# Kernel optimization log

Hardware: AMD Instinct MI355X
Metric: run time of the kernel (lower is better)

The kernel has to match this reference:

```python
import jax, jax.numpy as jnp
import numpy as np

C = 256
CQK = C // 8  # query/key projection dim (in_dim // 8)
B, H, W = 4, 64, 64


def setup_inputs() -> dict:
    key = jax.random.key(0)
    ks = jax.random.split(key, 7)
    scale = 0.05
    x = jax.random.normal(ks[0], (B, C, H, W), dtype=jnp.float32)
    Wq = jax.random.normal(ks[1], (CQK, C), dtype=jnp.float32) * scale
    bq = jax.random.normal(ks[2], (CQK,), dtype=jnp.float32) * scale
    Wk = jax.random.normal(ks[3], (CQK, C), dtype=jnp.float32) * scale
    bk = jax.random.normal(ks[4], (CQK,), dtype=jnp.float32) * scale
    Wv = jax.random.normal(ks[5], (C, C), dtype=jnp.float32) * scale
    bv = jax.random.normal(ks[6], (C,), dtype=jnp.float32) * scale
    return {"x": x, "Wq": Wq, "bq": bq, "Wk": Wk, "bk": bk, "Wv": Wv, "bv": bv}


def reference(x, Wq, bq, Wk, bk, Wv, bv):
    b, c, h, w = x.shape
    n = h * w
    xf = x.reshape(b, c, n)  # [B, C, N]
    # 1x1 convs == per-pixel linear maps over channels
    q = jnp.einsum('dc,bcn->bnd', Wq, xf) + bq[None, None, :]   # [B, N, C/8]
    k = jnp.einsum('dc,bcn->bdn', Wk, xf) + bk[None, :, None]   # [B, C/8, N]
    v = jnp.einsum('dc,bcn->bdn', Wv, xf) + bv[None, :, None]   # [B, C, N]
    energy = jnp.einsum('bnd,bdm->bnm', q, k)                    # [B, N, N]
    attention = jax.nn.softmax(energy, axis=-1)                  # softmax over keys
    # out = V @ attention^T  (torch: bmm(proj_value, attention.permute(0,2,1)))
    out = jnp.einsum('bdm,bnm->bdn', v, attention)               # [B, C, N]
    return out.reshape(b, c, h, w) + x
```

## Files before the change

### kernel.cpp

```cpp
#include <hip/hip_runtime.h>
#include <math.h>

#define BATCH 4
#define CH    256
#define NPIX  4096
#define DQK   32

typedef short          s16;
typedef unsigned int   uint_t;
typedef __attribute__((ext_vector_type(8))) short short8;
typedef __attribute__((ext_vector_type(4))) float floatx4;
typedef __attribute__((ext_vector_type(16))) float floatx16;

__device__ __forceinline__ s16 f2bf(float f) {
  union { float f; uint_t u; } v; v.f = f;
  return (s16)((v.u + 0x8000u) >> 16);
}
__device__ __forceinline__ uint_t pk2(float a, float b) {
  union { float f; uint_t u; } x, y; x.f = a; y.f = b;
  return (((y.u + 0x8000u) >> 16) << 16) | ((x.u + 0x8000u) >> 16);
}

__global__ __launch_bounds__(256) void prepack(
    const float* __restrict__ Wq, const float* __restrict__ bq,
    const float* __restrict__ Wk, const float* __restrict__ bk,
    const float* __restrict__ Wv, const float* __restrict__ bv,
    s16* __restrict__ Wbf, float* __restrict__ Bsw)
{
  const int gid = blockIdx.x * 256 + threadIdx.x;
  const int e0  = gid * 4;
  const int row = e0 >> 8, col = e0 & 255;
  const float* src = (row < 32) ? Wq + (size_t)row * 256
                   : (row < 64) ? Wk + (size_t)(row - 32) * 256
                                : Wv + (size_t)(row - 64) * 256;
  float4 f = *(const float4*)(src + col);
  uint2 o; o.x = pk2(f.x, f.y); o.y = pk2(f.z, f.w);
  *(uint2*)(Wbf + e0) = o;
  if (gid < 320)
    Bsw[gid] = (gid < 32) ? bq[gid] : (gid < 64) ? bk[gid - 32] : bv[gid - 64];
}

__global__ __launch_bounds__(256, 2) void proj_mfma(
    const float* __restrict__ x, const s16* __restrict__ Wbf,
    const float* __restrict__ Bsw,
    s16* __restrict__ Qw, s16* __restrict__ Kw, s16* __restrict__ Vw)
{
  const int b  = blockIdx.x >> 7;
  const int n0 = (blockIdx.x & 127) << 5;
  const int t  = threadIdx.x;

  __shared__ s16 Xs[32][264];
  __shared__ s16 Os[256][40];

  const float* xb = x + (size_t)b * CH * NPIX + n0;
  #pragma unroll
  for (int i = 0; i < 2; ++i) {
    int task = i * 256 + t;
    int ncg  = task & 7;
    int kcg  = task >> 3;
    const float* src = xb + (size_t)(kcg * 4) * NPIX + ncg * 4;
    float rows[4][4];
    *(float4*)&rows[0][0] = *(const float4*)(src);
    *(float4*)&rows[1][0] = *(const float4*)(src + NPIX);
    *(float4*)&rows[2][0] = *(const float4*)(src + 2 * NPIX);
    *(float4*)&rows[3][0] = *(const float4*)(src + 3 * NPIX);
    #pragma unroll
    for (int c = 0; c < 4; ++c) {
      uint2 pk;
      pk.x = pk2(rows[0][c], rows[1][c]);
      pk.y = pk2(rows[2][c], rows[3][c]);
      *(uint2*)&Xs[ncg * 4 + c][kcg * 4] = pk;
    }
  }
  __syncthreads();

  const int w    = t >> 6;
  const int l15  = t & 15;
  const int quad = (t & 63) >> 4;

  floatx4 acc[5][2];
  #pragma unroll
  for (int si = 0; si < 5; ++si)
    #pragma unroll
    for (int nt = 0; nt < 2; ++nt) acc[si][nt] = (floatx4){0.f, 0.f, 0.f, 0.f};

  short8 afc[5], afn[5];
  #pragma unroll
  for (int si = 0; si < 5; ++si) {
    const int s = w + si * 4;
    afc[si] = *(const short8*)(Wbf + (size_t)(s * 16 + l15) * 256 + quad * 8);
  }
  for (int kc = 0; kc < 8; ++kc) {
    const int k0  = kc * 32;
    const int kn0 = (kc < 7) ? k0 + 32 : 0;
    #pragma unroll
    for (int si = 0; si < 5; ++si) {
      const int s = w + si * 4;
      afn[si] = *(const short8*)(Wbf + (size_t)(s * 16 + l15) * 256 + kn0 + quad * 8);
    }
    short8 bf[2];
    #pragma unroll
    for (int nt = 0; nt < 2; ++nt)
      bf[nt] = *(const short8*)&Xs[l15 + 16 * nt][k0 + quad * 8];
    #pragma unroll
    for (int si = 0; si < 5; ++si)
      #pragma unroll
      for (int nt = 0; nt < 2; ++nt)
        acc[si][nt] = __builtin_amdgcn_mfma_f32_16x16x32_bf16(afc[si], bf[nt], acc[si][nt], 0, 0, 0);
    #pragma unroll
    for (int si = 0; si < 5; ++si) afc[si] = afn[si];
  }

  #pragma unroll
  for (int si = 0; si < 5; ++si) {
    const int s = w + si * 4;
    float4 bb = *(const float4*)(Bsw + 16 * s + quad * 4);
    #pragma unroll
    for (int nt = 0; nt < 2; ++nt) {
      const int px  = 16 * nt + l15;
      float v0 = acc[si][nt][0] + bb.x;
      float v1 = acc[si][nt][1] + bb.y;
      float v2 = acc[si][nt][2] + bb.z;
      float v3 = acc[si][nt][3] + bb.w;
      if (s < 4) {
        s16* dst = (s < 2) ? Qw : Kw;
        int d0 = (s & 1) * 16 + quad * 4;
        uint2 pq; pq.x = pk2(v0, v1); pq.y = pk2(v2, v3);
        *(uint2*)(dst + ((size_t)b * NPIX + n0 + px) * DQK + d0) = pq;
      } else {
        const int c0 = (s - 4) * 16 + quad * 4;
        Os[c0 + 0][px] = f2bf(v0);
        Os[c0 + 1][px] = f2bf(v1);
        Os[c0 + 2][px] = f2bf(v2);
        Os[c0 + 3][px] = f2bf(v3);
      }
    }
  }
  __syncthreads();
  #pragma unroll
  for (int rep = 0; rep < 4; ++rep) {
    const int task = rep * 256 + t;
    const int ch   = task >> 2;
    const int seg  = task & 3;
    *(uint4*)(Vw + ((size_t)b * CH + ch) * NPIX + n0 + seg * 8) =
        *(const uint4*)&Os[ch][seg * 8];
  }
}

__global__ __launch_bounds__(512, 2) void attn_mfma(
    const s16* __restrict__ Qw, const s16* __restrict__ Kw,
    const s16* __restrict__ Vw, const float* __restrict__ x,
    float* __restrict__ out)
{
  const int bi = blockIdx.x;
  const int b  = bi & 3;
  const int qt = bi >> 2;
  const int n0 = qt * 64;
  const int t  = threadIdx.x;
  const int w    = t >> 6;
  const int l15  = t & 15;
  const int quad = (t & 63) >> 4;
  const int l31  = t & 31;
  const int lh   = (t & 63) >> 5;
  const int l7   = t & 7;
  const int cb   = 32 * w;

  __shared__ s16  Pt[2][64][128];
  __shared__ float Lsum[64][8];

  const s16* qbase = Qw + ((size_t)b * NPIX + n0) * DQK;
  short8 qb[4];
  #pragma unroll
  for (int tq = 0; tq < 4; ++tq)
    qb[tq] = *(const short8*)(qbase + (size_t)(16 * tq + l15) * DQK + quad * 8);

  floatx16 o[2];
  #pragma unroll
  for (int i = 0; i < 16; ++i) { o[0][i] = 0.f; o[1][i] = 0.f; }
  float l_part[4] = {0.f, 0.f, 0.f, 0.f};

  const s16* kbase = Kw + (size_t)b * NPIX * DQK;
  const s16* vbase = Vw + ((size_t)b * CH + cb) * NPIX;

  short8 ka_c, ka_n, va[8];
  ka_c = *(const short8*)(kbase + (size_t)(16 * w + l15) * DQK + quad * 8);
  #pragma unroll
  for (int ks = 0; ks < 8; ++ks)
    va[ks] = *(const short8*)(vbase + (size_t)l31 * NPIX + 16 * ks + 8 * lh);

  int buf = 0;
  for (int kt = 0; kt < 32; ++kt) {
    const int m0  = kt * 128;
    const int mn0 = (kt < 31) ? m0 + 128 : 0;

    floatx4 sacc[4];
    #pragma unroll
    for (int tq = 0; tq < 4; ++tq)
      sacc[tq] = __builtin_amdgcn_mfma_f32_16x16x32_bf16(
                   ka_c, qb[tq], (floatx4){0.f, 0.f, 0.f, 0.f}, 0, 0, 0);

    ka_n = *(const short8*)(kbase + (size_t)(mn0 + 16 * w + l15) * DQK + quad * 8);

    const int wslot = (((2 * w + (quad >> 1)) ^ l7) << 3) + (quad & 1) * 4;
    #pragma unroll
    for (int tq = 0; tq < 4; ++tq) {
      float p0 = __expf(fminf(sacc[tq][0], 60.f));
      float p1 = __expf(fminf(sacc[tq][1], 60.f));
      float p2 = __expf(fminf(sacc[tq][2], 60.f));
      float p3 = __expf(fminf(sacc[tq][3], 60.f));
      l_part[tq] += (p0 + p1) + (p2 + p3);
      uint2 pk; pk.x = pk2(p0, p1); pk.y = pk2(p2, p3);
      *(uint2*)&Pt[buf][16 * tq + l15][wslot] = pk;
    }
    __syncthreads();

    #pragma unroll
    for (int ks = 0; ks < 8; ++ks) {
      const int rslot = ((2 * ks + lh) ^ l7) << 3;
      short8 pb0 = *(const short8*)&Pt[buf][l31     ][rslot];
      short8 pb1 = *(const short8*)&Pt[buf][32 + l31][rslot];
      o[0] = __builtin_amdgcn_mfma_f32_32x32x16_bf16(va[ks], pb0, o[0], 0, 0, 0);
      o[1] = __builtin_amdgcn_mfma_f32_32x32x16_bf16(va[ks], pb1, o[1], 0, 0, 0);
    }
    #pragma unroll
    for (int ks = 0; ks < 8; ++ks)
      va[ks] = *(const short8*)(vbase + (size_t)l31 * NPIX + mn0 + 16 * ks + 8 * lh);

    ka_c = ka_n;
    buf ^= 1;
  }

  #pragma unroll
  for (int tq = 0; tq < 4; ++tq) {
    l_part[tq] += __shfl_xor(l_part[tq], 16);
    l_part[tq] += __shfl_xor(l_part[tq], 32);
  }
  if (quad == 0) {
    #pragma unroll
    for (int tq = 0; tq < 4; ++tq) Lsum[16 * tq + l15][w] = l_part[tq];
  }
  __syncthreads();

  #pragma unroll
  for (int half = 0; half < 2; ++half) {
    const int q = half * 32 + l31;
    float4 s0 = *(const float4*)&Lsum[q][0];
    float4 s1 = *(const float4*)&Lsum[q][4];
    float invq = 1.f / (((s0.x + s0.y) + (s0.z + s0.w)) +
                        ((s1.x + s1.y) + (s1.z + s1.w)));
    const int npx = n0 + q;
    #pragma unroll
    for (int r = 0; r < 16; ++r) {
      const int c = cb + (r & 3) + 8 * (r >> 2) + 4 * lh;
      const size_t off = ((size_t)b * CH + c) * NPIX + npx;
      out[off] = fmaf(o[half][r], invq, x[off]);
    }
  }
}

extern "C" void kernel_launch(void* const* d_in, const int* in_sizes, int n_in,
                              void* d_out, int out_size, void* d_ws, size_t ws_size,
                              hipStream_t stream) {
  (void)in_sizes; (void)n_in; (void)out_size; (void)ws_size;
  const float* x  = (const float*)d_in[0];
  const float* Wq = (const float*)d_in[1];
  const float* bq = (const float*)d_in[2];
  const float* Wk = (const float*)d_in[3];
  const float* bk = (const float*)d_in[4];
  const float* Wv = (const float*)d_in[5];
  const float* bv = (const float*)d_in[6];
  float* out = (float*)d_out;

  unsigned char* ws = (unsigned char*)d_ws;
  s16*   Qw  = (s16*)ws;
  s16*   Kw  = (s16*)(ws + (size_t)1 * 1024 * 1024);
  s16*   Vw  = (s16*)(ws + (size_t)2 * 1024 * 1024);
  s16*   Wbf = (s16*)(ws + (size_t)10 * 1024 * 1024);
  float* Bsw = (float*)(ws + (size_t)10 * 1024 * 1024 + 256 * 1024);

  hipLaunchKernelGGL(prepack, dim3(80), dim3(256), 0, stream,
                     Wq, bq, Wk, bk, Wv, bv, Wbf, Bsw);
  hipLaunchKernelGGL(proj_mfma, dim3(512), dim3(256), 0, stream,
                     x, Wbf, Bsw, Qw, Kw, Vw);
  hipLaunchKernelGGL(attn_mfma, dim3(256), dim3(512), 0, stream,
                     Qw, Kw, Vw, x, out);
}
```

Measured before the change: 158.1 us.

## Pre-tile V into MFMA fragment layout and split attention across 16 waves

```diff
diff --git a/kernel.cpp b/kernel.cpp
--- a/kernel.cpp
+++ b/kernel.cpp
@@ -140,16 +140,20 @@
   #pragma unroll
   for (int rep = 0; rep < 4; ++rep) {
     const int task = rep * 256 + t;
-    const int ch   = task >> 2;
-    const int seg  = task & 3;
-    *(uint4*)(Vw + ((size_t)b * CH + ch) * NPIX + n0 + seg * 8) =
-        *(const uint4*)&Os[ch][seg * 8];
-  }
-}
-
-__global__ __launch_bounds__(512, 2) void attn_mfma(
+    const int fid  = task >> 6;
+    const int ln   = task & 63;
+    const int c    = fid >> 1;
+    const int sl   = fid & 1;
+    const int row  = c * 32 + (ln & 31);
+    const int col  = sl * 16 + (ln >> 5) * 8;
+    *(uint4*)(Vw + (((size_t)b * 8 + c) * 256 + (n0 >> 4) + sl) * 512 + ln * 8) =
+        *(const uint4*)&Os[row][col];
+  }
+}
+
+__global__ __launch_bounds__(1024, 4) void attn_mfma(
     const s16* __restrict__ Qw, const s16* __restrict__ Kw,
-    const s16* __restrict__ Vw, const float* __restrict__ x,
+    const s16* __restrict__ Vt, const float* __restrict__ x,
     float* __restrict__ out)
 {
   const int bi = blockIdx.x;
@@ -158,92 +162,94 @@
   const int n0 = qt * 64;
   const int t  = threadIdx.x;
   const int w    = t >> 6;
+  const int lane = t & 63;
   const int l15  = t & 15;
-  const int quad = (t & 63) >> 4;
+  const int quad = lane >> 4;
   const int l31  = t & 31;
-  const int lh   = (t & 63) >> 5;
+  const int lh   = lane >> 5;
   const int l7   = t & 7;
-  const int cb   = 32 * w;
+  const int sw   = w & 7;
+  const int sq   = w >> 3;
+  const int c    = w >> 1;
+  const int qh   = w & 1;
 
   __shared__ s16  Pt[2][64][128];
   __shared__ float Lsum[64][8];
 
-  const s16* qbase = Qw + ((size_t)b * NPIX + n0) * DQK;
-  short8 qb[4];
-  #pragma unroll
-  for (int tq = 0; tq < 4; ++tq)
+  const s16* qbase = Qw + ((size_t)b * NPIX + n0 + sq * 32) * DQK;
+  short8 qb[2];
+  #pragma unroll
+  for (int tq = 0; tq < 2; ++tq)
     qb[tq] = *(const short8*)(qbase + (size_t)(16 * tq + l15) * DQK + quad * 8);
 
-  floatx16 o[2];
-  #pragma unroll
-  for (int i = 0; i < 16; ++i) { o[0][i] = 0.f; o[1][i] = 0.f; }
-  float l_part[4] = {0.f, 0.f, 0.f, 0.f};
+  floatx16 o;
+  #pragma unroll
+  for (int i = 0; i < 16; ++i) o[i] = 0.f;
+  float l_part[2] = {0.f, 0.f};
 
   const s16* kbase = Kw + (size_t)b * NPIX * DQK;
-  const s16* vbase = Vw + ((size_t)b * CH + cb) * NPIX;
+  const s16* vtb   = Vt + ((size_t)(b * 8 + c) * 256) * 512 + lane * 8;
 
   short8 ka_c, ka_n, va[8];
-  ka_c = *(const short8*)(kbase + (size_t)(16 * w + l15) * DQK + quad * 8);
+  ka_c = *(const short8*)(kbase + (size_t)(16 * sw + l15) * DQK + quad * 8);
   #pragma unroll
   for (int ks = 0; ks < 8; ++ks)
-    va[ks] = *(const short8*)(vbase + (size_t)l31 * NPIX + 16 * ks + 8 * lh);
+    va[ks] = *(const short8*)(vtb + (size_t)ks * 512);
 
   int buf = 0;
   for (int kt = 0; kt < 32; ++kt) {
     const int m0  = kt * 128;
     const int mn0 = (kt < 31) ? m0 + 128 : 0;
 
-    floatx4 sacc[4];
-    #pragma unroll
-    for (int tq = 0; tq < 4; ++tq)
+    floatx4 sacc[2];
+    #pragma unroll
+    for (int tq = 0; tq < 2; ++tq)
       sacc[tq] = __builtin_amdgcn_mfma_f32_16x16x32_bf16(
                    ka_c, qb[tq], (floatx4){0.f, 0.f, 0.f, 0.f}, 0, 0, 0);
 
-    ka_n = *(const short8*)(kbase + (size_t)(mn0 + 16 * w + l15) * DQK + quad * 8);
-
-    const int wslot = (((2 * w + (quad >> 1)) ^ l7) << 3) + (quad & 1) * 4;
-    #pragma unroll
-    for (int tq = 0; tq < 4; ++tq) {
+    ka_n = *(const short8*)(kbase + (size_t)(mn0 + 16 * sw + l15) * DQK + quad * 8);
+
+    const int wslot = (((2 * sw + (quad >> 1)) ^ l7) << 3) + (quad & 1) * 4;
+    #pragma unroll
+    for (int tq = 0; tq < 2; ++tq) {
       float p0 = __expf(fminf(sacc[tq][0], 60.f));
       float p1 = __expf(fminf(sacc[tq][1], 60.f));
       float p2 = __expf(fminf(sacc[tq][2], 60.f));
       float p3 = __expf(fminf(sacc[tq][3], 60.f));
       l_part[tq] += (p0 + p1) + (p2 + p3);
       uint2 pk; pk.x = pk2(p0, p1); pk.y = pk2(p2, p3);
-      *(uint2*)&Pt[buf][16 * tq + l15][wslot] = pk;
+      *(uint2*)&Pt[buf][sq * 32 + 16 * tq + l15][wslot] = pk;
     }
     __syncthreads();
 
     #pragma unroll
     for (int ks = 0; ks < 8; ++ks) {
       const int rslot = ((2 * ks + lh) ^ l7) << 3;
-      short8 pb0 = *(const short8*)&Pt[buf][l31     ][rslot];
-      short8 pb1 = *(const short8*)&Pt[buf][32 + l31][rslot];
-      o[0] = __builtin_amdgcn_mfma_f32_32x32x16_bf16(va[ks], pb0, o[0], 0, 0, 0);
-      o[1] = __builtin_amdgcn_mfma_f32_32x32x16_bf16(va[ks], pb1, o[1], 0, 0, 0);
-    }
+      short8 pb = *(const short8*)&Pt[buf][qh * 32 + l31][rslot];
+      o = __builtin_amdgcn_mfma_f32_32x32x16_bf16(va[ks], pb, o, 0, 0, 0);
+    }
+    const int sn = mn0 >> 4;
     #pragma unroll
     for (int ks = 0; ks < 8; ++ks)
-      va[ks] = *(const short8*)(vbase + (size_t)l31 * NPIX + mn0 + 16 * ks + 8 * lh);
+      va[ks] = *(const short8*)(vtb + (size_t)(sn + ks) * 512);
 
     ka_c = ka_n;
     buf ^= 1;
   }
 
   #pragma unroll
-  for (int tq = 0; tq < 4; ++tq) {
+  for (int tq = 0; tq < 2; ++tq) {
     l_part[tq] += __shfl_xor(l_part[tq], 16);
     l_part[tq] += __shfl_xor(l_part[tq], 32);
   }
   if (quad == 0) {
     #pragma unroll
-    for (int tq = 0; tq < 4; ++tq) Lsum[16 * tq + l15][w] = l_part[tq];
+    for (int tq = 0; tq < 2; ++tq) Lsum[sq * 32 + 16 * tq + l15][sw] = l_part[tq];
   }
   __syncthreads();
 
-  #pragma unroll
-  for (int half = 0; half < 2; ++half) {
-    const int q = half * 32 + l31;
+  {
+    const int q = qh * 32 + l31;
     float4 s0 = *(const float4*)&Lsum[q][0];
     float4 s1 = *(const float4*)&Lsum[q][4];
     float invq = 1.f / (((s0.x + s0.y) + (s0.z + s0.w)) +
@@ -251,9 +257,9 @@
     const int npx = n0 + q;
     #pragma unroll
     for (int r = 0; r < 16; ++r) {
-      const int c = cb + (r & 3) + 8 * (r >> 2) + 4 * lh;
-      const size_t off = ((size_t)b * CH + c) * NPIX + npx;
-      out[off] = fmaf(o[half][r], invq, x[off]);
+      const int ch = c * 32 + (r & 3) + 8 * (r >> 2) + 4 * lh;
+      const size_t off = ((size_t)b * CH + ch) * NPIX + npx;
+      out[off] = fmaf(o[r], invq, x[off]);
     }
   }
 }
@@ -274,14 +280,14 @@
   unsigned char* ws = (unsigned char*)d_ws;
   s16*   Qw  = (s16*)ws;
   s16*   Kw  = (s16*)(ws + (size_t)1 * 1024 * 1024);
-  s16*   Vw  = (s16*)(ws + (size_t)2 * 1024 * 1024);
+  s16*   Vt  = (s16*)(ws + (size_t)2 * 1024 * 1024);
   s16*   Wbf = (s16*)(ws + (size_t)10 * 1024 * 1024);
   float* Bsw = (float*)(ws + (size_t)10 * 1024 * 1024 + 256 * 1024);
 
   hipLaunchKernelGGL(prepack, dim3(80), dim3(256), 0, stream,
                      Wq, bq, Wk, bk, Wv, bv, Wbf, Bsw);
   hipLaunchKernelGGL(proj_mfma, dim3(512), dim3(256), 0, stream,
-                     x, Wbf, Bsw, Qw, Kw, Vw);
-  hipLaunchKernelGGL(attn_mfma, dim3(256), dim3(512), 0, stream,
-                     Qw, Kw, Vw, x, out);
-}
+                     x, Wbf, Bsw, Qw, Kw, Vt);
+  hipLaunchKernelGGL(attn_mfma, dim3(256), dim3(1024), 0, stream,
+                     Qw, Kw, Vt, x, out);
+}
```

After: 147.5 us. 6.7% less time.
